# Optimization experiments

Measured on AMD Instinct MI355X. Metric: run time of the kernel, lower is better.

Reference implementation:

```python
import jax, jax.numpy as jnp
import numpy as np

D_MODEL = 1024
NUM_HEADS = 16
D_K = D_MODEL // NUM_HEADS
FFN_SIZE = 4096
EPS = 1e-6


def _layer_norm(x, gamma, beta):
    mu = jnp.mean(x, axis=-1, keepdims=True)
    var = jnp.var(x, axis=-1, keepdims=True)
    return (x - mu) / jnp.sqrt(var + EPS) * gamma + beta


def setup_inputs() -> dict:
    key = jax.random.key(0)
    ks = jax.random.split(key, 12)
    B, S = 2, 2048
    s_attn = 1.0 / np.sqrt(D_MODEL)
    s_ffn1 = 1.0 / np.sqrt(D_MODEL)
    s_ffn2 = 1.0 / np.sqrt(FFN_SIZE)
    return {
        "x": jax.random.normal(ks[0], (B, S, D_MODEL), dtype=jnp.float32),
        "W_q": jax.random.normal(ks[1], (D_MODEL, D_MODEL), dtype=jnp.float32) * s_attn,
        "W_k": jax.random.normal(ks[2], (D_MODEL, D_MODEL), dtype=jnp.float32) * s_attn,
        "W_v": jax.random.normal(ks[3], (D_MODEL, D_MODEL), dtype=jnp.float32) * s_attn,
        "W_o": jax.random.normal(ks[4], (D_MODEL, D_MODEL), dtype=jnp.float32) * s_attn,
        "b_o": jnp.zeros((D_MODEL,), dtype=jnp.float32),
        "W1": jax.random.normal(ks[5], (D_MODEL, FFN_SIZE), dtype=jnp.float32) * s_ffn1,
        "b1": jnp.zeros((FFN_SIZE,), dtype=jnp.float32),
        "W2": jax.random.normal(ks[6], (FFN_SIZE, D_MODEL), dtype=jnp.float32) * s_ffn2,
        "b2": jnp.zeros((D_MODEL,), dtype=jnp.float32),
        "ln1_g": jnp.ones((D_MODEL,), dtype=jnp.float32),
        "ln1_b": jnp.zeros((D_MODEL,), dtype=jnp.float32),
        "ln2_g": jnp.ones((D_MODEL,), dtype=jnp.float32),
        "ln2_b": jnp.zeros((D_MODEL,), dtype=jnp.float32),
    }


def reference(x, W_q, W_k, W_v, W_o, b_o, W1, b1, W2, b2,
              ln1_g, ln1_b, ln2_g, ln2_b):
    B, S, _ = x.shape

    # --- self-attention sublayer (pre-norm residual) ---
    h = _layer_norm(x, ln1_g, ln1_b)
    q = (h @ W_q).reshape(B, S, NUM_HEADS, D_K).transpose(0, 2, 1, 3)  # [B,H,S,Dk]
    k = (h @ W_k).reshape(B, S, NUM_HEADS, D_K).transpose(0, 2, 1, 3)
    v = (h @ W_v).reshape(B, S, NUM_HEADS, D_K).transpose(0, 2, 1, 3)
    scores = jnp.einsum("bhqd,bhkd->bhqk", q, k) / jnp.sqrt(jnp.float32(D_K))
    attn = jax.nn.softmax(scores, axis=-1)
    ctx = jnp.einsum("bhqk,bhkd->bhqd", attn, v)
    ctx = ctx.transpose(0, 2, 1, 3).reshape(B, S, D_MODEL)
    x = x + (ctx @ W_o + b_o)

    # --- FFN sublayer (pre-norm residual) ---
    h2 = _layer_norm(x, ln2_g, ln2_b)
    f = jax.nn.relu(h2 @ W1 + b1) @ W2 + b2
    return x + f
```

## Files before the change

kernel.cpp:

```cpp
#include <hip/hip_runtime.h>
#include <cstdint>
#include <cstddef>


typedef __attribute__((ext_vector_type(8))) __bf16 bf16x8;
typedef __attribute__((ext_vector_type(4))) __bf16 bf16x4;
typedef __attribute__((ext_vector_type(4))) float f32x4;

__device__ __forceinline__ void async16(const void* g, void* l) {
  __builtin_amdgcn_global_load_lds(
      (__attribute__((address_space(1))) void*)g,
      (__attribute__((address_space(3))) void*)l, 16, 0, 0);
}

__device__ __forceinline__ f32x4 mfma16(bf16x8 a, bf16x8 b, f32x4 c) {
  return __builtin_amdgcn_mfma_f32_16x16x32_bf16(a, b, c, 0, 0, 0);
}

template <int N>
__device__ __forceinline__ void wait_vmcnt() {
  if constexpr (N == 0) {
    asm volatile("s_waitcnt vmcnt(0)" ::: "memory");
  } else if constexpr (N == 3) {
    asm volatile("s_waitcnt vmcnt(3)" ::: "memory");
  } else {
    asm volatile("s_waitcnt vmcnt(4)" ::: "memory");
  }
}
__device__ __forceinline__ void barrier_raw() {
  asm volatile("s_barrier" ::: "memory");
}
__device__ __forceinline__ void lgkm0() {
  asm volatile("s_waitcnt lgkmcnt(0)" ::: "memory");
}

__device__ __forceinline__ void ln_body(const float* __restrict__ xin,
                                        const float* __restrict__ g,
                                        const float* __restrict__ bt,
                                        __bf16* __restrict__ out, int tok,
                                        int lane) {
  const int base0 = lane * 8, base1 = 512 + lane * 8;
  const float* xr = xin + (size_t)tok * 1024;
  float v[16];
  float4 a0 = *(const float4*)(xr + base0);
  float4 a1 = *(const float4*)(xr + base0 + 4);
  float4 a2 = *(const float4*)(xr + base1);
  float4 a3 = *(const float4*)(xr + base1 + 4);
  v[0] = a0.x; v[1] = a0.y; v[2] = a0.z; v[3] = a0.w;
  v[4] = a1.x; v[5] = a1.y; v[6] = a1.z; v[7] = a1.w;
  v[8] = a2.x; v[9] = a2.y; v[10] = a2.z; v[11] = a2.w;
  v[12] = a3.x; v[13] = a3.y; v[14] = a3.z; v[15] = a3.w;
  float s = 0.f, s2 = 0.f;
#pragma unroll
  for (int i = 0; i < 16; i++) { s += v[i]; s2 += v[i] * v[i]; }
#pragma unroll
  for (int m = 1; m < 64; m <<= 1) {
    s += __shfl_xor(s, m);
    s2 += __shfl_xor(s2, m);
  }
  const float mean = s * (1.f / 1024.f);
  const float var = s2 * (1.f / 1024.f) - mean * mean;
  const float rstd = rsqrtf(var + 1e-6f);
  float4 g0 = *(const float4*)(g + base0), g1 = *(const float4*)(g + base0 + 4);
  float4 g2 = *(const float4*)(g + base1), g3 = *(const float4*)(g + base1 + 4);
  float4 b0 = *(const float4*)(bt + base0), b1v = *(const float4*)(bt + base0 + 4);
  float4 b2v = *(const float4*)(bt + base1), b3 = *(const float4*)(bt + base1 + 4);
  float gg[16] = {g0.x, g0.y, g0.z, g0.w, g1.x, g1.y, g1.z, g1.w,
                  g2.x, g2.y, g2.z, g2.w, g3.x, g3.y, g3.z, g3.w};
  float bb[16] = {b0.x, b0.y, b0.z, b0.w, b1v.x, b1v.y, b1v.z, b1v.w,
                  b2v.x, b2v.y, b2v.z, b2v.w, b3.x, b3.y, b3.z, b3.w};
  bf16x8 o0, o1;
#pragma unroll
  for (int j = 0; j < 8; j++) {
    o0[j] = (__bf16)((v[j] - mean) * rstd * gg[j] + bb[j]);
    o1[j] = (__bf16)((v[8 + j] - mean) * rstd * gg[8 + j] + bb[8 + j]);
  }
  __bf16* op = out + (size_t)tok * 1024;
  *(bf16x8*)(op + base0) = o0;
  *(bf16x8*)(op + base1) = o1;
}

__global__ __launch_bounds__(256) void prep_kernel(
    const float* __restrict__ Wq, const float* __restrict__ Wk,
    const float* __restrict__ Wv, const float* __restrict__ Wo,
    const float* __restrict__ W1, const float* __restrict__ W2,
    const float* __restrict__ x, const float* __restrict__ ln1g,
    const float* __restrict__ ln1b, __bf16* __restrict__ WqkvT,
    __bf16* __restrict__ WoT, __bf16* __restrict__ W1T,
    __bf16* __restrict__ W2T, __bf16* __restrict__ h) {
  const int id = blockIdx.x;
  if (id >= 3072) {
    const int tok = (id - 3072) * 4 + (threadIdx.x >> 6);
    ln_body(x, ln1g, ln1b, h, tok, threadIdx.x & 63);
    return;
  }
  const float* in;
  __bf16* out;
  int ld_in, ld_out, c0, r0;
  if (id < 1024) {
    const int which = id >> 8, tl = id & 255;
    c0 = (tl & 15) * 64;
    r0 = (tl >> 4) * 64;
    ld_in = 1024;
    ld_out = 1024;
    if (which == 0) { in = Wq; out = WqkvT; }
    else if (which == 1) { in = Wk; out = WqkvT + 1048576; }
    else if (which == 2) { in = Wv; out = WqkvT + 2097152; }
    else { in = Wo; out = WoT; }
  } else if (id < 2048) {
    const int tl = id - 1024;
    c0 = (tl & 63) * 64;
    r0 = (tl >> 6) * 64;
    in = W1; out = W1T; ld_in = 4096; ld_out = 1024;
  } else {
    const int tl = id - 2048;
    c0 = (tl & 15) * 64;
    r0 = (tl >> 4) * 64;
    in = W2; out = W2T; ld_in = 1024; ld_out = 4096;
  }
  __shared__ __bf16 tile[64][65];
  const int tx = threadIdx.x & 63, ty = threadIdx.x >> 6;
#pragma unroll
  for (int i = 0; i < 16; i++) {
    int r = ty + i * 4;
    tile[r][tx] = (__bf16)in[(size_t)(r0 + r) * ld_in + c0 + tx];
  }
  __syncthreads();
#pragma unroll
  for (int i = 0; i < 16; i++) {
    int r = ty + i * 4;
    out[(size_t)(c0 + r) * ld_out + r0 + tx] = tile[tx][r];
  }
}

__global__ __launch_bounds__(256) void ln_kernel(
    const float* __restrict__ xin, const float* __restrict__ g,
    const float* __restrict__ bt, __bf16* __restrict__ out) {
  const int tok = blockIdx.x * 4 + (threadIdx.x >> 6);
  ln_body(xin, g, bt, out, tok, threadIdx.x & 63);
}

__global__ __launch_bounds__(256) void transpose_vt_perm(
    const unsigned short* __restrict__ in, unsigned short* __restrict__ out,
    int ld_in, int ld_out) {
  __shared__ unsigned short tile[64][65];
  const int c0 = blockIdx.x * 64, r0 = blockIdx.y * 64;
  const int tx = threadIdx.x & 63, ty = threadIdx.x >> 6;
#pragma unroll
  for (int i = 0; i < 16; i++) {
    int r = ty + i * 4;
    tile[r][tx] = in[(size_t)(r0 + r) * ld_in + c0 + tx];
  }
  __syncthreads();
  const int ptx = (tx & 32) + 2 * (tx & 15) + ((tx >> 4) & 1);
#pragma unroll
  for (int i = 0; i < 16; i++) {
    int r = ty + i * 4;
    out[(size_t)(c0 + r) * ld_out + r0 + ptx] = tile[tx][r];
  }
}

template <int EPI, int SPLITS = 1>
__global__ __launch_bounds__(512, 2) void gemm256(
    const __bf16* __restrict__ A, int lda, const __bf16* __restrict__ BT,
    int ldb, void* __restrict__ C, int ldc, int Kb,
    const float* __restrict__ bias) {
  const int t = threadIdx.x;
  const int m0 = blockIdx.x * 256, n0 = blockIdx.y * 256;
  const int kz = (SPLITS > 1) ? blockIdx.z : 0;
  __shared__ __align__(16) __bf16 As[2][2][8192];
  __shared__ __align__(16) __bf16 Bs[2][2][8192];
  const int lane = t & 63;
  const int quad = lane >> 4, l15 = lane & 15;
  const int w = t >> 6, wm = w >> 2, wn = w & 3;

  f32x4 acc[8][4] = {};

  const int rr = t >> 3;
  const int ca = (t & 7) ^ (rr & 7);
  const int cc = rr & 31;
  const int wnb = t >> 8;
  const int cb = (t & 7) ^ (cc & 7);
  const __bf16* gA = A + (size_t)kz * Kb + (size_t)(m0 + rr) * lda + ca * 8;
  const __bf16* gB = BT + (size_t)kz * Kb +
                     (size_t)(n0 + wnb * 64 + cc) * ldb + cb * 8;
  const size_t a64 = (size_t)64 * lda, a128 = (size_t)128 * lda;
  const size_t b32 = (size_t)32 * ldb, b128 = (size_t)128 * ldb;

  auto stageA = [&](int buf, int mq, int ko) {
    const __bf16* g = gA + (mq ? a64 : 0) + ko;
    __bf16* l = &As[buf][mq][t * 8];
    async16(g, l);
    async16(g + a128, l + 4096);
  };
  auto stageB = [&](int buf, int nq, int ko) {
    const __bf16* g = gB + (nq ? b32 : 0) + ko;
    __bf16* l = &Bs[buf][nq][t * 8];
    async16(g, l);
    async16(g + b128, l + 4096);
  };

  const int arow = wm * 4096 + l15 * 64;
  const int brow = wn * 2048 + l15 * 64;
  const int x7 = l15 & 7;

  auto loadA = [&](int buf, int mq, bf16x8 (&af)[4][2]) {
#pragma unroll
    for (int mi = 0; mi < 4; mi++)
#pragma unroll
      for (int kk = 0; kk < 2; kk++)
        af[mi][kk] = *(const bf16x8*)&As[buf][mq]
            [arow + mi * 1024 + (((kk * 4 + quad) ^ x7) * 8)];
  };
  auto loadB = [&](int buf, int nq, bf16x8 (&bv)[2][2]) {
#pragma unroll
    for (int ni = 0; ni < 2; ni++)
#pragma unroll
      for (int kk = 0; kk < 2; kk++)
        bv[ni][kk] = *(const bf16x8*)&Bs[buf][nq]
            [brow + ni * 1024 + (((kk * 4 + quad) ^ x7) * 8)];
  };
  auto mm = [&](int mq, int nq, const bf16x8 (&af)[4][2],
                const bf16x8 (&bv)[2][2]) {
    __builtin_amdgcn_s_setprio(1);
#pragma unroll
    for (int mi = 0; mi < 4; mi++)
#pragma unroll
      for (int ni = 0; ni < 2; ni++)
#pragma unroll
        for (int kk = 0; kk < 2; kk++)
          acc[mq * 4 + mi][nq * 2 + ni] =
              mfma16(af[mi][kk], bv[ni][kk], acc[mq * 4 + mi][nq * 2 + ni]);
    __builtin_amdgcn_s_setprio(0);
  };

  const int NT = Kb / 64;
  stageA(0, 0, 0); stageB(0, 0, 0); stageA(0, 1, 0); stageB(0, 1, 0);
  stageA(1, 0, 64); stageB(1, 0, 64);
  wait_vmcnt<4>();
  barrier_raw();

  bf16x8 af[4][2], b0[2][2], b1[2][2];
  for (int s = 0; s < NT; ++s) {
    const int buf = s & 1;
    const int ko1 = (s + 1) * 64, ko2 = (s + 2) * 64;
    loadA(buf, 0, af);
    loadB(buf, 0, b0);
    if (s + 1 < NT) stageA(buf ^ 1, 1, ko1);
    barrier_raw();
    lgkm0();
    mm(0, 0, af, b0);
    barrier_raw();
    loadB(buf, 1, b1);
    if (s + 1 < NT) stageB(buf ^ 1, 1, ko1);
    barrier_raw();
    lgkm0();
    mm(0, 1, af, b1);
    barrier_raw();
    loadA(buf, 1, af);
    if (s + 2 < NT) stageA(buf, 0, ko2);
    barrier_raw();
    lgkm0();
    mm(1, 0, af, b0);
    barrier_raw();
    if (s + 2 < NT) {
      stageB(buf, 0, ko2);
      wait_vmcnt<4>();
    } else {
      wait_vmcnt<0>();
    }
    barrier_raw();
    mm(1, 1, af, b1);
    barrier_raw();
  }

  float biasv[4];
  if constexpr (EPI == 2) {
#pragma unroll
    for (int ni = 0; ni < 4; ni++)
      biasv[ni] = bias[n0 + wn * 64 + ni * 16 + l15];
  }
  __bf16* Cb = (__bf16*)C;
  if constexpr (SPLITS > 1)
    Cb += (size_t)kz * (size_t)gridDim.x * 256 * ldc;
#pragma unroll
  for (int mi = 0; mi < 8; mi++)
#pragma unroll
    for (int ni = 0; ni < 4; ni++)
#pragma unroll
      for (int r = 0; r < 4; r++) {
        const int row = m0 + wm * 128 + mi * 16 + quad * 4 + r;
        const int col = n0 + wn * 64 + ni * 16 + l15;
        float v = acc[mi][ni][r];
        if constexpr (EPI == 0) {
          Cb[(size_t)row * ldc + col] = (__bf16)v;
        } else {
          v += biasv[ni];
          Cb[(size_t)row * ldc + col] = (__bf16)fmaxf(v, 0.f);
        }
      }
}

template <int EPI, int TM, int SPLITS = 1>
__global__ __launch_bounds__(256) void gemm_bt(
    const __bf16* __restrict__ A, int lda, const __bf16* __restrict__ BT,
    int ldb, void* __restrict__ C, int ldc, int Kb,
    const float* __restrict__ bias, const float* __restrict__ res, int ldres) {
  const int t = threadIdx.x;
  const int m0 = blockIdx.x * TM, n0 = blockIdx.y * 128;
  const int kz = (SPLITS > 1) ? blockIdx.z : 0;
  __shared__ __align__(16) __bf16 As[3][TM * 32];
  __shared__ __align__(16) __bf16 Bs[3][128 * 32];
  const int lane = t & 63, w = t >> 6;
  const int quad = lane >> 4, l15 = lane & 15;
  const int wm = w >> 1, wn = w & 1;
  constexpr int MF = TM / 32;
  constexpr int LOADS = TM / 64 + 2;

  f32x4 acc[MF][4] = {};

  const int swc = ((t & 3) ^ ((t >> 3) & 3)) * 8;
  const __bf16* ga = A + (size_t)(m0 + (t >> 2)) * lda + swc + (size_t)kz * Kb;
  const __bf16* gb = BT + (size_t)(n0 + (t >> 2)) * ldb + swc + (size_t)kz * Kb;
  const size_t a64 = (size_t)64 * lda, b64 = (size_t)64 * ldb;

  auto stage = [&](int buf) {
#pragma unroll
    for (int i = 0; i < TM / 64; i++)
      async16(ga + i * a64, As[buf] + t * 8 + i * 2048);
    async16(gb, Bs[buf] + t * 8);
    async16(gb + b64, Bs[buf] + t * 8 + 2048);
    ga += 32;
    gb += 32;
  };
  const int ce = (quad ^ ((l15 >> 1) & 3)) * 8;
  auto compute = [&](int buf) {
    bf16x8 af[MF], bfr[4];
#pragma unroll
    for (int i = 0; i < MF; i++)
      af[i] = *(const bf16x8*)&As[buf][(wm * (TM / 2) + i * 16 + l15) * 32 + ce];
#pragma unroll
    for (int i = 0; i < 4; i++)
      bfr[i] = *(const bf16x8*)&Bs[buf][(wn * 64 + i * 16 + l15) * 32 + ce];
#pragma unroll
    for (int mi = 0; mi < MF; mi++)
#pragma unroll
      for (int ni = 0; ni < 4; ni++)
        acc[mi][ni] = mfma16(af[mi], bfr[ni], acc[mi][ni]);
  };

  const int iters = Kb / 32;
  stage(0);
  stage(1);
  int cur = 0, stg = 2;
  for (int it = 0; it < iters - 1; ++it) {
    wait_vmcnt<LOADS>();
    barrier_raw();
    if (it + 2 < iters) stage(stg);
    compute(cur);
    cur = (cur == 2) ? 0 : cur + 1;
    stg = (stg == 2) ? 0 : stg + 1;
  }
  wait_vmcnt<0>();
  barrier_raw();
  compute(cur);

  float biasv[4];
  if constexpr (EPI != 0) {
#pragma unroll
    for (int ni = 0; ni < 4; ni++)
      biasv[ni] = bias[n0 + wn * 64 + ni * 16 + l15];
  }
  __bf16* Cb = (__bf16*)C;
  if constexpr (SPLITS > 1)
    Cb += (size_t)kz * gridDim.x * TM * ldc;
#pragma unroll
  for (int mi = 0; mi < MF; mi++)
#pragma unroll
    for (int ni = 0; ni < 4; ni++)
#pragma unroll
      for (int r = 0; r < 4; r++) {
        const int row = m0 + wm * (TM / 2) + mi * 16 + quad * 4 + r;
        const int col = n0 + wn * 64 + ni * 16 + l15;
        float v = acc[mi][ni][r];
        if constexpr (EPI == 0) {
          Cb[(size_t)row * ldc + col] = (__bf16)v;
        } else if constexpr (EPI == 1) {
          v += biasv[ni] + res[(size_t)row * ldres + col];
          ((float*)C)[(size_t)row * ldc + col] = v;
        } else {
          v += biasv[ni];
          ((__bf16*)C)[(size_t)row * ldc + col] = (__bf16)fmaxf(v, 0.f);
        }
      }
}

__global__ __launch_bounds__(256) void reduce_split4(
    const __bf16* __restrict__ P, const float* __restrict__ bias,
    const float* __restrict__ res, float* __restrict__ out) {
  const int row = blockIdx.x, c = threadIdx.x * 4;
  const size_t i = (size_t)row * 1024 + c;
  float4 r = *(const float4*)(res + i);
  float4 bv = *(const float4*)(bias + c);
  float s0 = r.x + bv.x, s1 = r.y + bv.y, s2 = r.z + bv.z, s3 = r.w + bv.w;
#pragma unroll
  for (int j = 0; j < 4; j++) {
    bf16x4 p = *(const bf16x4*)(P + (size_t)j * 4194304 + i);
    s0 += (float)p[0];
    s1 += (float)p[1];
    s2 += (float)p[2];
    s3 += (float)p[3];
  }
  float4 o = {s0, s1, s2, s3};
  *(float4*)(out + i) = o;
}

__global__ __launch_bounds__(256, 2) void attn_kernel(
    const __bf16* __restrict__ QKV, const __bf16* __restrict__ VT,
    __bf16* __restrict__ ctx) {
  const int id = blockIdx.x;
  const int xg = id & 7, idx = id >> 3;
  const int bh = xg * 4 + (idx & 3);
  const int qt = idx >> 2;
  const int b = bh >> 4, h = bh & 15;
  const int t = threadIdx.x, w = t >> 6, lane = t & 63;
  const int quad = lane >> 4, l15 = lane & 15;
  const int tok0 = b * 2048;
  const int q0w = tok0 + qt * 128 + w * 32;

  __shared__ __align__(16) __bf16 Ks[2][128 * 64];
  __shared__ __align__(16) __bf16 VTs[2][64 * 128];

  const float qs = 0.18033688011112042f;
  bf16x8 qf[2][2];
#pragma unroll
  for (int mi = 0; mi < 2; mi++)
#pragma unroll
    for (int kb = 0; kb < 2; kb++) {
      const __bf16* src = QKV + (size_t)(q0w + mi * 16 + l15) * 3072 + h * 64 +
                          kb * 32 + quad * 8;
      bf16x8 r = *(const bf16x8*)src;
#pragma unroll
      for (int j = 0; j < 8; j++) r[j] = (__bf16)((float)r[j] * qs);
      qf[mi][kb] = r;
    }

  f32x4 lacc[2] = {};
  f32x4 O[2][4] = {};

  const int krow = t >> 3;
  const int kcg = (((t & 7) ^ (krow & 7)) * 8);
  const int vrow = t >> 4;
  const int vcg = (((2 * (t & 15)) ^ ((vrow & 7) * 2)) * 4);
  const int x7 = l15 & 7;

  auto stage = [&](int buf, int kt) {
    const int ktok = tok0 + kt * 128;
#pragma unroll
    for (int j = 0; j < 4; j++) {
      const __bf16* gp =
          QKV + (size_t)(ktok + krow + j * 32) * 3072 + 1024 + h * 64 + kcg;
      async16(gp, Ks[buf] + t * 8 + j * 2048);
    }
#pragma unroll
    for (int j = 0; j < 4; j++) {
      const __bf16* gp =
          VT + (size_t)(h * 64 + vrow + j * 16) * 4096 + ktok + vcg;
      async16(gp, VTs[buf] + t * 8 + j * 2048);
    }
  };

  stage(0, 0);
  wait_vmcnt<0>();
  barrier_raw();

  int buf = 0;
  for (int kt = 0; kt < 16; ++kt) {
    if (kt + 1 < 16) stage(buf ^ 1, kt + 1);

    f32x4 sT[2][8];
    __builtin_amdgcn_s_setprio(1);
#pragma unroll
    for (int kt8 = 0; kt8 < 8; kt8++) {
      f32x4 a0 = {}, a1 = {};
#pragma unroll
      for (int kb = 0; kb < 2; kb++) {
        bf16x8 kf = *(const bf16x8*)&Ks[buf][(kt8 * 16 + l15) * 64 +
                                            (((kb * 4 + quad) ^ x7) * 8)];
        a0 = mfma16(kf, qf[0][kb], a0);
        a1 = mfma16(kf, qf[1][kb], a1);
      }
      sT[0][kt8] = a0;
      sT[1][kt8] = a1;
    }
    __builtin_amdgcn_s_setprio(0);

#pragma unroll
    for (int kb = 0; kb < 4; kb++) {
      bf16x8 pf0, pf1;
#pragma unroll
      for (int hf = 0; hf < 2; hf++)
#pragma unroll
        for (int r = 0; r < 4; r++) {
          const float p0 = __builtin_amdgcn_exp2f(sT[0][2 * kb + hf][r]);
          const float p1 = __builtin_amdgcn_exp2f(sT[1][2 * kb + hf][r]);
          lacc[0][r] += p0;
          lacc[1][r] += p1;
          pf0[r * 2 + hf] = (__bf16)p0;
          pf1[r * 2 + hf] = (__bf16)p1;
        }
      __builtin_amdgcn_s_setprio(1);
#pragma unroll
      for (int nd = 0; nd < 4; nd++) {
        bf16x8 vf = *(const bf16x8*)&VTs[buf][(nd * 16 + l15) * 128 +
                                             (((4 * kb + quad) ^ x7) * 8)];
        O[0][nd] = mfma16(pf0, vf, O[0][nd]);
        O[1][nd] = mfma16(pf1, vf, O[1][nd]);
      }
      __builtin_amdgcn_s_setprio(0);
    }

    wait_vmcnt<0>();
    barrier_raw();
    buf ^= 1;
  }

#pragma unroll
  for (int mi = 0; mi < 2; mi++) {
    float lsum = lacc[mi][0] + lacc[mi][1] + lacc[mi][2] + lacc[mi][3];
    lsum += __shfl_xor(lsum, 16);
    lsum += __shfl_xor(lsum, 32);
    float rl[4];
#pragma unroll
    for (int r = 0; r < 4; r++) rl[r] = 1.0f / __shfl(lsum, quad * 4 + r);
#pragma unroll
    for (int nd = 0; nd < 4; nd++)
#pragma unroll
      for (int r = 0; r < 4; r++) {
        const int tokq = q0w + mi * 16 + quad * 4 + r;
        const int col = h * 64 + nd * 16 + l15;
        ctx[(size_t)tokq * 1024 + col] = (__bf16)(O[mi][nd][r] * rl[r]);
      }
  }
}

extern "C" void kernel_launch(void* const* d_in, const int* in_sizes, int n_in,
                              void* d_out, int out_size, void* d_ws,
                              size_t ws_size, hipStream_t stream) {
  (void)in_sizes; (void)n_in; (void)out_size; (void)ws_size;

  const float* x = (const float*)d_in[0];
  const float* Wq = (const float*)d_in[1];
  const float* Wk = (const float*)d_in[2];
  const float* Wv = (const float*)d_in[3];
  const float* Wo = (const float*)d_in[4];
  const float* b_o = (const float*)d_in[5];
  const float* W1 = (const float*)d_in[6];
  const float* b1 = (const float*)d_in[7];
  const float* W2 = (const float*)d_in[8];
  const float* b2 = (const float*)d_in[9];
  const float* ln1g = (const float*)d_in[10];
  const float* ln1b = (const float*)d_in[11];
  const float* ln2g = (const float*)d_in[12];
  const float* ln2b = (const float*)d_in[13];

  char* ws = (char*)d_ws;
  __bf16* h = (__bf16*)(ws + 0);
  __bf16* W1T = (__bf16*)(ws + 8388608);
  __bf16* WqkvT = (__bf16*)(ws + 16777216);
  __bf16* WoT = (__bf16*)(ws + 23068672);
  __bf16* QKV = (__bf16*)(ws + 25165824);
  __bf16* VT = (__bf16*)(ws + 50331648);
  __bf16* ctx = (__bf16*)(ws + 58720256);
  __bf16* f1 = (__bf16*)(ws + 33554432);
  __bf16* Pw2 = (__bf16*)(ws + 0);
  float* x1 = (float*)(ws + 67108864);
  __bf16* W2T = (__bf16*)(ws + 83886080);

  const dim3 blk(256);
  const dim3 blk512(512);

  prep_kernel<<<dim3(4096), blk, 0, stream>>>(Wq, Wk, Wv, Wo, W1, W2, x, ln1g,
                                              ln1b, WqkvT, WoT, W1T, W2T, h);

  gemm256<0><<<dim3(16, 12), blk512, 0, stream>>>(
      h, 1024, WqkvT, 1024, (void*)QKV, 3072, 1024, nullptr);

  transpose_vt_perm<<<dim3(16, 64), blk, 0, stream>>>(
      (const unsigned short*)(QKV + 2048), (unsigned short*)VT, 3072, 4096);

  attn_kernel<<<dim3(512), blk, 0, stream>>>(QKV, VT, ctx);

  gemm_bt<1, 64><<<dim3(64, 8), blk, 0, stream>>>(
      ctx, 1024, WoT, 1024, (void*)x1, 1024, 1024, b_o, x, 1024);

  ln_kernel<<<dim3(1024), blk, 0, stream>>>(x1, ln2g, ln2b, h);

  gemm256<2><<<dim3(16, 16), blk512, 0, stream>>>(
      h, 1024, W1T, 1024, (void*)f1, 4096, 1024, b1);

  gemm256<0, 4><<<dim3(16, 4, 4), blk512, 0, stream>>>(
      f1, 4096, W2T, 4096, (void*)Pw2, 1024, 1024, nullptr);
  reduce_split4<<<dim3(4096), blk, 0, stream>>>(Pw2, b2, x1, (float*)d_out);
}
```

Baseline: 309.2 us.

## Fuse V transpose into QKV GEMM epilogue and read V directly from global

```diff
diff --git a/kernel.cpp b/kernel.cpp
--- a/kernel.cpp
+++ b/kernel.cpp
@@ -140,31 +140,11 @@
   ln_body(xin, g, bt, out, tok, threadIdx.x & 63);
 }
 
-__global__ __launch_bounds__(256) void transpose_vt_perm(
-    const unsigned short* __restrict__ in, unsigned short* __restrict__ out,
-    int ld_in, int ld_out) {
-  __shared__ unsigned short tile[64][65];
-  const int c0 = blockIdx.x * 64, r0 = blockIdx.y * 64;
-  const int tx = threadIdx.x & 63, ty = threadIdx.x >> 6;
-#pragma unroll
-  for (int i = 0; i < 16; i++) {
-    int r = ty + i * 4;
-    tile[r][tx] = in[(size_t)(r0 + r) * ld_in + c0 + tx];
-  }
-  __syncthreads();
-  const int ptx = (tx & 32) + 2 * (tx & 15) + ((tx >> 4) & 1);
-#pragma unroll
-  for (int i = 0; i < 16; i++) {
-    int r = ty + i * 4;
-    out[(size_t)(c0 + r) * ld_out + r0 + ptx] = tile[tx][r];
-  }
-}
-
 template <int EPI, int SPLITS = 1>
 __global__ __launch_bounds__(512, 2) void gemm256(
     const __bf16* __restrict__ A, int lda, const __bf16* __restrict__ BT,
     int ldb, void* __restrict__ C, int ldc, int Kb,
-    const float* __restrict__ bias) {
+    const float* __restrict__ bias, __bf16* __restrict__ VTout) {
   const int t = threadIdx.x;
   const int m0 = blockIdx.x * 256, n0 = blockIdx.y * 256;
   const int kz = (SPLITS > 1) ? blockIdx.z : 0;
@@ -274,6 +254,25 @@
     barrier_raw();
   }
 
+  if constexpr (EPI == 3) {
+    if (n0 >= 2048) {
+      const int colb = m0 + wm * 128;
+#pragma unroll
+      for (int mi = 0; mi < 8; mi++) {
+        const int tcol = colb + (mi >> 1) * 32 + quad * 8 + (mi & 1) * 4;
+#pragma unroll
+        for (int ni = 0; ni < 4; ni++) {
+          const int vrow = n0 - 2048 + wn * 64 + ni * 16 + l15;
+          bf16x4 o;
+#pragma unroll
+          for (int r = 0; r < 4; r++) o[r] = (__bf16)acc[mi][ni][r];
+          *(bf16x4*)&VTout[(size_t)vrow * 4096 + tcol] = o;
+        }
+      }
+      return;
+    }
+  }
+
   float biasv[4];
   if constexpr (EPI == 2) {
 #pragma unroll
@@ -292,7 +291,7 @@
         const int row = m0 + wm * 128 + mi * 16 + quad * 4 + r;
         const int col = n0 + wn * 64 + ni * 16 + l15;
         float v = acc[mi][ni][r];
-        if constexpr (EPI == 0) {
+        if constexpr (EPI == 0 || EPI == 3) {
           Cb[(size_t)row * ldc + col] = (__bf16)v;
         } else {
           v += biasv[ni];
@@ -415,7 +414,7 @@
   *(float4*)(out + i) = o;
 }
 
-__global__ __launch_bounds__(256, 2) void attn_kernel(
+__global__ __launch_bounds__(256, 3) void attn_kernel(
     const __bf16* __restrict__ QKV, const __bf16* __restrict__ VT,
     __bf16* __restrict__ ctx) {
   const int id = blockIdx.x;
@@ -429,7 +428,6 @@
   const int q0w = tok0 + qt * 128 + w * 32;
 
   __shared__ __align__(16) __bf16 Ks[2][128 * 64];
-  __shared__ __align__(16) __bf16 VTs[2][64 * 128];
 
   const float qs = 0.18033688011112042f;
   bf16x8 qf[2][2];
@@ -450,9 +448,8 @@
 
   const int krow = t >> 3;
   const int kcg = (((t & 7) ^ (krow & 7)) * 8);
-  const int vrow = t >> 4;
-  const int vcg = (((2 * (t & 15)) ^ ((vrow & 7) * 2)) * 4);
   const int x7 = l15 & 7;
+  const __bf16* vbase = VT + (size_t)(h * 64 + l15) * 4096 + tok0;
 
   auto stage = [&](int buf, int kt) {
     const int ktok = tok0 + kt * 128;
@@ -462,12 +459,6 @@
           QKV + (size_t)(ktok + krow + j * 32) * 3072 + 1024 + h * 64 + kcg;
       async16(gp, Ks[buf] + t * 8 + j * 2048);
     }
-#pragma unroll
-    for (int j = 0; j < 4; j++) {
-      const __bf16* gp =
-          VT + (size_t)(h * 64 + vrow + j * 16) * 4096 + ktok + vcg;
-      async16(gp, VTs[buf] + t * 8 + j * 2048);
-    }
   };
 
   stage(0, 0);
@@ -477,6 +468,7 @@
   int buf = 0;
   for (int kt = 0; kt < 16; ++kt) {
     if (kt + 1 < 16) stage(buf ^ 1, kt + 1);
+    const int ko = kt * 128;
 
     f32x4 sT[2][8];
     __builtin_amdgcn_s_setprio(1);
@@ -497,6 +489,11 @@
 
 #pragma unroll
     for (int kb = 0; kb < 4; kb++) {
+      bf16x8 vf[4];
+#pragma unroll
+      for (int nd = 0; nd < 4; nd++)
+        vf[nd] = *(const bf16x8*)&vbase[(size_t)(nd * 16) * 4096 + ko +
+                                        (4 * kb + quad) * 8];
       bf16x8 pf0, pf1;
 #pragma unroll
       for (int hf = 0; hf < 2; hf++)
@@ -506,16 +503,14 @@
           const float p1 = __builtin_amdgcn_exp2f(sT[1][2 * kb + hf][r]);
           lacc[0][r] += p0;
           lacc[1][r] += p1;
-          pf0[r * 2 + hf] = (__bf16)p0;
-          pf1[r * 2 + hf] = (__bf16)p1;
+          pf0[hf * 4 + r] = (__bf16)p0;
+          pf1[hf * 4 + r] = (__bf16)p1;
         }
       __builtin_amdgcn_s_setprio(1);
 #pragma unroll
       for (int nd = 0; nd < 4; nd++) {
-        bf16x8 vf = *(const bf16x8*)&VTs[buf][(nd * 16 + l15) * 128 +
-                                             (((4 * kb + quad) ^ x7) * 8)];
-        O[0][nd] = mfma16(pf0, vf, O[0][nd]);
-        O[1][nd] = mfma16(pf1, vf, O[1][nd]);
+        O[0][nd] = mfma16(pf0, vf[nd], O[0][nd]);
+        O[1][nd] = mfma16(pf1, vf[nd], O[1][nd]);
       }
       __builtin_amdgcn_s_setprio(0);
     }
@@ -583,11 +578,8 @@
   prep_kernel<<<dim3(4096), blk, 0, stream>>>(Wq, Wk, Wv, Wo, W1, W2, x, ln1g,
                                               ln1b, WqkvT, WoT, W1T, W2T, h);
 
-  gemm256<0><<<dim3(16, 12), blk512, 0, stream>>>(
-      h, 1024, WqkvT, 1024, (void*)QKV, 3072, 1024, nullptr);
-
-  transpose_vt_perm<<<dim3(16, 64), blk, 0, stream>>>(
-      (const unsigned short*)(QKV + 2048), (unsigned short*)VT, 3072, 4096);
+  gemm256<3><<<dim3(16, 12), blk512, 0, stream>>>(
+      h, 1024, WqkvT, 1024, (void*)QKV, 3072, 1024, nullptr, VT);
 
   attn_kernel<<<dim3(512), blk, 0, stream>>>(QKV, VT, ctx);
 
@@ -597,9 +589,9 @@
   ln_kernel<<<dim3(1024), blk, 0, stream>>>(x1, ln2g, ln2b, h);
 
   gemm256<2><<<dim3(16, 16), blk512, 0, stream>>>(
-      h, 1024, W1T, 1024, (void*)f1, 4096, 1024, b1);
+      h, 1024, W1T, 1024, (void*)f1, 4096, 1024, b1, nullptr);
 
   gemm256<0, 4><<<dim3(16, 4, 4), blk512, 0, stream>>>(
-      f1, 4096, W2T, 4096, (void*)Pw2, 1024, 1024, nullptr);
+      f1, 4096, W2T, 4096, (void*)Pw2, 1024, 1024, nullptr, nullptr);
   reduce_split4<<<dim3(4096), blk, 0, stream>>>(Pw2, b2, x1, (float*)d_out);
 }
```

New measurement: 393.3 us. 27.2% more time.
